# Optimization experiments

Measured on AMD Instinct MI355X. Metric: run time of the kernel, lower is better.

The kernel has to match this reference:

```python
import jax, jax.numpy as jnp
import numpy as np

B, M, ND, ED, D, H = 4, 1024, 64, 8, 64, 4
ALPHA = 0.2
NEG = -9.0e15


def setup_inputs() -> dict:
    key = jax.random.key(0)
    ks = jax.random.split(key, 6)
    h = jax.random.normal(ks[0], (B, M, ND), jnp.float32)
    mch_mask = jax.random.randint(ks[1], (B, M, M), 0, 2).astype(jnp.int32)
    comp_val = jax.random.normal(ks[2], (B, M, M, ED), jnp.float32)
    W = jax.random.normal(ks[3], (H, ND, D), jnp.float32) * 0.1
    W_edge = jax.random.normal(ks[4], (H, ED, D), jnp.float32) * 0.1
    a = jax.random.normal(ks[5], (H, 3 * D), jnp.float32) * 0.1
    return {"h": h, "mch_mask": mch_mask, "comp_val": comp_val,
            "W": W, "W_edge": W_edge, "a": a}


def reference(h, mch_mask, comp_val, W, W_edge, a):
    # h: [B,M,ND], mch_mask: [B,M,M], comp_val: [B,M,M,ED]
    # W: [H,ND,D], W_edge: [H,ED,D], a: [H,3D]  (heads stacked)
    d = W.shape[-1]
    a1, a2, a3 = a[:, :d], a[:, d:2 * d], a[:, 2 * d:]
    Wh = jnp.einsum('bmd,hde->bhme', h, W)              # [B,H,M,D]
    Wh1 = jnp.einsum('bhme,he->bhm', Wh, a1)            # [B,H,M]
    Wh2 = jnp.einsum('bhme,he->bhm', Wh, a2)            # [B,H,M]
    # edge_feas = (comp_val @ W_edge) @ a3, fused: comp_val @ (W_edge @ a3)
    w_e = jnp.einsum('hed,hd->he', W_edge, a3)          # [H,ED]
    edge_feas = jnp.einsum('bkqe,he->bhkq', comp_val, w_e)  # [B,H,M,M]
    e = Wh1[:, :, :, None] + Wh2[:, :, None, :] + edge_feas
    e = jnp.where(e > 0, e, ALPHA * e)                  # leaky_relu
    e = jnp.where(mch_mask[:, None, :, :] > 0, e, NEG)
    attn = jax.nn.softmax(e, axis=-1)                   # [B,H,M,M]
    h_prime = jnp.einsum('bhkq,bhqd->bhkd', attn, Wh)   # [B,H,M,D]
    b, nh, m, dd = h_prime.shape
    return h_prime.transpose(0, 2, 1, 3).reshape(b, m, nh * dd)  # concat heads
```

## Files before the change

### kernel.cpp

```cpp
#include <hip/hip_runtime.h>
#include <hip/hip_bf16.h>

typedef float v4f __attribute__((ext_vector_type(4)));

#define B_ 4
#define M_ 1024
#define ND_ 64
#define ED_ 8
#define D_ 64
#define H_ 4
#define KT 8
#define QC 64
#define NCH (M_ / QC)
#define ALPHA 0.2f

#define WS_WH1 1048576
#define WS_WH2 1064960

#define WHL_F (QC * 256)
#define PB_H 520
#define PB_F (H_ * PB_H)
#define LDS_BYTES ((WHL_F + PB_F + 32 + 32) * 4)

__device__ __forceinline__ v4f splat(float s) { return (v4f){s, s, s, s}; }

__device__ __forceinline__ v4f f4fma(v4f a, v4f b, v4f c) {
#if __has_builtin(__builtin_elementwise_fma)
    return __builtin_elementwise_fma(a, b, c);
#else
    v4f r;
    r.x = fmaf(a.x, b.x, c.x);
    r.y = fmaf(a.y, b.y, c.y);
    r.z = fmaf(a.z, b.z, c.z);
    r.w = fmaf(a.w, b.w, c.w);
    return r;
#endif
}

__global__ __launch_bounds__(256) void k_pre(const float* __restrict__ hg,
                                             const float* __restrict__ Wg,
                                             const float* __restrict__ ag,
                                             float* __restrict__ Whg,
                                             float* __restrict__ Wh1g,
                                             float* __restrict__ Wh2g) {
    __shared__ float wl[ND_ * D_];
    __shared__ float hl[16 * 68];
    const int t = threadIdx.x, lane = t & 63, wv = t >> 6;
    const int bid = blockIdx.x;
    const int b = bid >> 8, h = (bid >> 6) & (H_ - 1), mb = bid & 63;
    const int m0 = mb * 16;

    {
        const float* wsrc = Wg + h * ND_ * D_;
#pragma unroll
        for (int i = 0; i < 4; ++i) {
            const float* s = wsrc + (wv * 4 + i) * 256 + lane * 4;
            __builtin_amdgcn_global_load_lds(
                (const __attribute__((address_space(1))) void*)s,
                (__attribute__((address_space(3))) void*)(wl + (wv * 4 + i) * 256), 16, 0, 0);
        }
    }
    {
        const int mh = t >> 4, u = t & 15;
        v4f hv = *(const v4f*)(hg + ((size_t)(b * M_) + m0 + mh) * ND_ + u * 4);
        *(v4f*)(hl + mh * 68 + u * 4) = hv;
    }
    __syncthreads();

    const int m = t >> 4, d4 = t & 15;
    v4f acc = {0.f, 0.f, 0.f, 0.f};
#pragma unroll
    for (int i = 0; i < ND_; ++i) {
        v4f w4 = *(const v4f*)(wl + i * 64 + d4 * 4);
        float hs = hl[m * 68 + i];
        acc = f4fma(splat(hs), w4, acc);
    }
    *(v4f*)(Whg + (((size_t)(b * H_ + h)) * M_ + m0 + m) * D_ + d4 * 4) = acc;

    v4f a1 = *(const v4f*)(ag + h * 192 + d4 * 4);
    v4f a2 = *(const v4f*)(ag + h * 192 + 64 + d4 * 4);
    v4f p1 = acc * a1, p2 = acc * a2;
    float r1 = (p1.x + p1.y) + (p1.z + p1.w);
    float r2 = (p2.x + p2.y) + (p2.z + p2.w);
#pragma unroll
    for (int off = 8; off >= 1; off >>= 1) {
        r1 += __shfl_xor(r1, off);
        r2 += __shfl_xor(r2, off);
    }
    if (d4 == 0) {
        Wh1g[((size_t)(b * H_ + h)) * M_ + m0 + m] = r1;
        Wh2g[((size_t)(b * H_ + h)) * M_ + m0 + m] = r2;
    }
}

__global__ __launch_bounds__(512, 4) void k_main(const float* __restrict__ cvg,
                                                 const int* __restrict__ mg,
                                                 const float* __restrict__ Whg,
                                                 const float* __restrict__ Wh1g,
                                                 const float* __restrict__ Wh2g,
                                                 const float* __restrict__ Weg,
                                                 const float* __restrict__ ag,
                                                 float* __restrict__ outg) {
    extern __shared__ float smem[];
    float* whl = smem;
    float* pb = smem + WHL_F;
    float* wel = pb + PB_F;
    float* sl = wel + 32;

    const int t = threadIdx.x, lane = t & 63, wv = t >> 6;
    const int nid = (blockIdx.x & 7) * 64 + (blockIdx.x >> 3);
    const int b = nid >> 7;
    const int k0 = (nid & 127) * KT;
    const int hh = lane >> 4, d4 = lane & 15;

    if (t < 32) {
        const int h = t >> 3, e = t & 7;
        const float* wrow = Weg + (h * ED_ + e) * D_;
        const float* a3 = ag + h * 192 + 128;
        float a = 0.f;
#pragma unroll
        for (int i = 0; i < D_; ++i) a = fmaf(wrow[i], a3[i], a);
        wel[t] = a;
    }

    const int ek = k0 + wv;
    float wh1r[H_];
#pragma unroll
    for (int h = 0; h < H_; ++h) wh1r[h] = Wh1g[(b * H_ + h) * M_ + ek];

    const v4f* cvrow = (const v4f*)(cvg + (size_t)(b * M_ + ek) * M_ * ED_);
    const int* mrow = mg + (size_t)(b * M_ + ek) * M_;

    v4f acc[KT];
#pragma unroll
    for (int k = 0; k < KT; ++k) acc[k] = (v4f){0.f, 0.f, 0.f, 0.f};
    float sreg[H_] = {0.f, 0.f, 0.f, 0.f};

#pragma unroll
    for (int i = 0; i < KT; ++i) {
        const int q = wv * KT + i;
        const float* src = Whg + ((size_t)(b * H_ + hh) * M_ + q) * D_ + d4 * 4;
        __builtin_amdgcn_global_load_lds((const __attribute__((address_space(1))) void*)src,
                                         (__attribute__((address_space(3))) void*)(whl + q * 256),
                                         16, 0, 0);
    }
    v4f cv0 = cvrow[lane * 2], cv1 = cvrow[lane * 2 + 1];
    int mk = mrow[lane];
    float wh2r[H_];
#pragma unroll
    for (int h = 0; h < H_; ++h) wh2r[h] = Wh2g[(b * H_ + h) * M_ + lane];
    __syncthreads();

    for (int c = 0; c < NCH; ++c) {
#pragma unroll
        for (int h = 0; h < H_; ++h) {
            v4f wa = *(const v4f*)(wel + h * 8);
            v4f wb = *(const v4f*)(wel + h * 8 + 4);
            v4f tt = cv0 * wa + cv1 * wb;
            float ef = (tt.x + tt.y) + (tt.z + tt.w);
            float e = wh1r[h] + wh2r[h] + ef;
            e = fmaxf(e, ALPHA * e);
            float p = (mk > 0) ? __expf(e) : 0.0f;
            pb[h * PB_H + wv * QC + lane] = p;
            sreg[h] += p;
        }
        __syncthreads();

        if (c + 1 < NCH) {
            const int qn = (c + 1) * QC + lane;
            cv0 = cvrow[qn * 2];
            cv1 = cvrow[qn * 2 + 1];
            mk = mrow[qn];
#pragma unroll
            for (int h = 0; h < H_; ++h) wh2r[h] = Wh2g[(b * H_ + h) * M_ + qn];
        }

        {
            const int q0 = wv * 8;
#pragma unroll
            for (int qq = 0; qq < 2; ++qq) {
                const int q = q0 + qq * 4;
                const v4f w0 = *(const v4f*)(whl + (q + 0) * 256 + lane * 4);
                const v4f w1 = *(const v4f*)(whl + (q + 1) * 256 + lane * 4);
                const v4f w2 = *(const v4f*)(whl + (q + 2) * 256 + lane * 4);
                const v4f w3 = *(const v4f*)(whl + (q + 3) * 256 + lane * 4);
                const float* pbase = pb + hh * PB_H + q;
#pragma unroll
                for (int k = 0; k < KT; ++k) {
                    const v4f pq = *(const v4f*)(pbase + k * 64);
                    v4f a = acc[k];
                    a = f4fma(splat(pq.x), w0, a);
                    a = f4fma(splat(pq.y), w1, a);
                    a = f4fma(splat(pq.z), w2, a);
                    a = f4fma(splat(pq.w), w3, a);
                    acc[k] = a;
                }
            }
        }
        __syncthreads();

        if (c + 1 < NCH) {
#pragma unroll
            for (int i = 0; i < KT; ++i) {
                const int q = wv * KT + i;
                const float* src =
                    Whg + ((size_t)(b * H_ + hh) * M_ + (c + 1) * QC + q) * D_ + d4 * 4;
                __builtin_amdgcn_global_load_lds(
                    (const __attribute__((address_space(1))) void*)src,
                    (__attribute__((address_space(3))) void*)(whl + q * 256), 16, 0, 0);
            }
        }
    }

#pragma unroll
    for (int h = 0; h < H_; ++h) {
        float r = sreg[h];
#pragma unroll
        for (int off = 32; off >= 1; off >>= 1) r += __shfl_xor(r, off);
        if (lane == 0) sl[wv * H_ + h] = r;
    }
#pragma unroll
    for (int k = 0; k < KT; ++k)
        *(v4f*)(whl + (wv * KT + k) * 256 + lane * 4) = acc[k];
    __syncthreads();
    {
        v4f r = (v4f){0.f, 0.f, 0.f, 0.f};
#pragma unroll
        for (int p = 0; p < 8; ++p)
            r += *(const v4f*)(whl + (p * KT + wv) * 256 + lane * 4);
        const float inv = 1.0f / sl[wv * H_ + hh];
        r *= splat(inv);
        *(v4f*)(outg + (size_t)(b * M_ + k0 + wv) * (H_ * D_) + lane * 4) = r;
    }
}

extern "C" void kernel_launch(void* const* d_in, const int* in_sizes, int n_in,
                              void* d_out, int out_size, void* d_ws, size_t ws_size,
                              hipStream_t stream) {
    const float* hg = (const float*)d_in[0];
    const int* mg = (const int*)d_in[1];
    const float* cvg = (const float*)d_in[2];
    const float* Wg = (const float*)d_in[3];
    const float* Weg = (const float*)d_in[4];
    const float* ag = (const float*)d_in[5];
    float* outg = (float*)d_out;
    float* ws = (float*)d_ws;
    float* Whg = ws;
    float* Wh1g = ws + WS_WH1;
    float* Wh2g = ws + WS_WH2;

    (void)hipFuncSetAttribute((const void*)k_main,
                              hipFuncAttributeMaxDynamicSharedMemorySize, LDS_BYTES);

    k_pre<<<1024, 256, 0, stream>>>(hg, Wg, ag, Whg, Wh1g, Wh2g);
    k_main<<<512, 512, LDS_BYTES, stream>>>(cvg, mg, Whg, Wh1g, Wh2g, Weg, ag, outg);
}
```

Baseline: 252.6 us.

## Read Wh directly from global into registers and double-buffer probability LDS

Stops staging Wh tiles in LDS through async global_load_lds. Each thread now loads its eight Wh rows straight from global/L2 into registers every chunk. The probability buffer is double-buffered, which removes one __syncthreads per chunk. Wh1/Wh2 are stored head-minor so a single v4f load fetches all four heads, and the final cross-wave reduction uses a smaller scratch in two passes to shrink LDS. The trade-off is redundant global loads of Wh across waves, plus possible extra latency that is no longer hidden by LDS prefetch.

```diff
diff --git a/kernel.cpp b/kernel.cpp
--- a/kernel.cpp
+++ b/kernel.cpp
@@ -17,10 +17,8 @@
 #define WS_WH1 1048576
 #define WS_WH2 1064960
 
-#define WHL_F (QC * 256)
 #define PB_H 520
 #define PB_F (H_ * PB_H)
-#define LDS_BYTES ((WHL_F + PB_F + 32 + 32) * 4)
 
 __device__ __forceinline__ v4f splat(float s) { return (v4f){s, s, s, s}; }
 
@@ -88,8 +86,8 @@
         r2 += __shfl_xor(r2, off);
     }
     if (d4 == 0) {
-        Wh1g[((size_t)(b * H_ + h)) * M_ + m0 + m] = r1;
-        Wh2g[((size_t)(b * H_ + h)) * M_ + m0 + m] = r2;
+        Wh1g[((size_t)(b * M_) + m0 + m) * H_ + h] = r1;
+        Wh2g[((size_t)(b * M_) + m0 + m) * H_ + h] = r2;
     }
 }
 
@@ -101,11 +99,10 @@
                                                  const float* __restrict__ Weg,
                                                  const float* __restrict__ ag,
                                                  float* __restrict__ outg) {
-    extern __shared__ float smem[];
-    float* whl = smem;
-    float* pb = smem + WHL_F;
-    float* wel = pb + PB_F;
-    float* sl = wel + 32;
+    __shared__ float pb[2 * PB_F];
+    __shared__ float scr[32 * 256];
+    __shared__ float wel[32];
+    __shared__ float sl[32];
 
     const int t = threadIdx.x, lane = t & 63, wv = t >> 6;
     const int nid = (blockIdx.x & 7) * 64 + (blockIdx.x >> 3);
@@ -124,44 +121,34 @@
     }
 
     const int ek = k0 + wv;
-    float wh1r[H_];
-#pragma unroll
-    for (int h = 0; h < H_; ++h) wh1r[h] = Wh1g[(b * H_ + h) * M_ + ek];
-
+    const v4f wh1r = *(const v4f*)(Wh1g + (size_t)(b * M_ + ek) * H_);
     const v4f* cvrow = (const v4f*)(cvg + (size_t)(b * M_ + ek) * M_ * ED_);
     const int* mrow = mg + (size_t)(b * M_ + ek) * M_;
+    const int q0 = wv * 8;
+    const float* whb = Whg + ((size_t)(b * H_ + hh) * M_) * D_ + d4 * 4;
 
     v4f acc[KT];
 #pragma unroll
     for (int k = 0; k < KT; ++k) acc[k] = (v4f){0.f, 0.f, 0.f, 0.f};
     float sreg[H_] = {0.f, 0.f, 0.f, 0.f};
 
-#pragma unroll
-    for (int i = 0; i < KT; ++i) {
-        const int q = wv * KT + i;
-        const float* src = Whg + ((size_t)(b * H_ + hh) * M_ + q) * D_ + d4 * 4;
-        __builtin_amdgcn_global_load_lds((const __attribute__((address_space(1))) void*)src,
-                                         (__attribute__((address_space(3))) void*)(whl + q * 256),
-                                         16, 0, 0);
-    }
     v4f cv0 = cvrow[lane * 2], cv1 = cvrow[lane * 2 + 1];
     int mk = mrow[lane];
-    float wh2r[H_];
-#pragma unroll
-    for (int h = 0; h < H_; ++h) wh2r[h] = Wh2g[(b * H_ + h) * M_ + lane];
+    v4f wh2v = *(const v4f*)(Wh2g + (size_t)(b * M_ + lane) * H_);
     __syncthreads();
 
     for (int c = 0; c < NCH; ++c) {
+        float* pbw = pb + (c & 1) * PB_F;
 #pragma unroll
         for (int h = 0; h < H_; ++h) {
             v4f wa = *(const v4f*)(wel + h * 8);
             v4f wb = *(const v4f*)(wel + h * 8 + 4);
             v4f tt = cv0 * wa + cv1 * wb;
             float ef = (tt.x + tt.y) + (tt.z + tt.w);
-            float e = wh1r[h] + wh2r[h] + ef;
+            float e = wh1r[h] + wh2v[h] + ef;
             e = fmaxf(e, ALPHA * e);
             float p = (mk > 0) ? __expf(e) : 0.0f;
-            pb[h * PB_H + wv * QC + lane] = p;
+            pbw[h * PB_H + wv * QC + lane] = p;
             sreg[h] += p;
         }
         __syncthreads();
@@ -171,45 +158,29 @@
             cv0 = cvrow[qn * 2];
             cv1 = cvrow[qn * 2 + 1];
             mk = mrow[qn];
-#pragma unroll
-            for (int h = 0; h < H_; ++h) wh2r[h] = Wh2g[(b * H_ + h) * M_ + qn];
+            wh2v = *(const v4f*)(Wh2g + (size_t)(b * M_ + qn) * H_);
         }
 
         {
-            const int q0 = wv * 8;
+            const float* whc = whb + (size_t)(c * QC + q0) * D_;
+            v4f w[8];
+#pragma unroll
+            for (int j = 0; j < 8; ++j) w[j] = *(const v4f*)(whc + (size_t)j * D_);
+            const float* pbr = pbw + hh * PB_H + q0;
 #pragma unroll
             for (int qq = 0; qq < 2; ++qq) {
-                const int q = q0 + qq * 4;
-                const v4f w0 = *(const v4f*)(whl + (q + 0) * 256 + lane * 4);
-                const v4f w1 = *(const v4f*)(whl + (q + 1) * 256 + lane * 4);
-                const v4f w2 = *(const v4f*)(whl + (q + 2) * 256 + lane * 4);
-                const v4f w3 = *(const v4f*)(whl + (q + 3) * 256 + lane * 4);
-                const float* pbase = pb + hh * PB_H + q;
 #pragma unroll
                 for (int k = 0; k < KT; ++k) {
-                    const v4f pq = *(const v4f*)(pbase + k * 64);
+                    const v4f pq = *(const v4f*)(pbr + k * QC + qq * 4);
                     v4f a = acc[k];
-                    a = f4fma(splat(pq.x), w0, a);
-                    a = f4fma(splat(pq.y), w1, a);
-                    a = f4fma(splat(pq.z), w2, a);
-                    a = f4fma(splat(pq.w), w3, a);
+                    a = f4fma(splat(pq.x), w[qq * 4 + 0], a);
+                    a = f4fma(splat(pq.y), w[qq * 4 + 1], a);
+                    a = f4fma(splat(pq.z), w[qq * 4 + 2], a);
+                    a = f4fma(splat(pq.w), w[qq * 4 + 3], a);
                     acc[k] = a;
                 }
             }
         }
-        __syncthreads();
-
-        if (c + 1 < NCH) {
-#pragma unroll
-            for (int i = 0; i < KT; ++i) {
-                const int q = wv * KT + i;
-                const float* src =
-                    Whg + ((size_t)(b * H_ + hh) * M_ + (c + 1) * QC + q) * D_ + d4 * 4;
-                __builtin_amdgcn_global_load_lds(
-                    (const __attribute__((address_space(1))) void*)src,
-                    (__attribute__((address_space(3))) void*)(whl + q * 256), 16, 0, 0);
-            }
-        }
     }
 
 #pragma unroll
@@ -220,16 +191,26 @@
         if (lane == 0) sl[wv * H_ + h] = r;
     }
 #pragma unroll
-    for (int k = 0; k < KT; ++k)
-        *(v4f*)(whl + (wv * KT + k) * 256 + lane * 4) = acc[k];
-    __syncthreads();
-    {
+    for (int k = 0; k < 4; ++k) *(v4f*)(scr + (wv * 4 + k) * 256 + lane * 4) = acc[k];
+    __syncthreads();
+    if (wv < 4) {
         v4f r = (v4f){0.f, 0.f, 0.f, 0.f};
 #pragma unroll
         for (int p = 0; p < 8; ++p)
-            r += *(const v4f*)(whl + (p * KT + wv) * 256 + lane * 4);
-        const float inv = 1.0f / sl[wv * H_ + hh];
-        r *= splat(inv);
+            r += *(const v4f*)(scr + (p * 4 + wv) * 256 + lane * 4);
+        r *= splat(1.0f / sl[wv * H_ + hh]);
+        *(v4f*)(outg + (size_t)(b * M_ + k0 + wv) * (H_ * D_) + lane * 4) = r;
+    }
+    __syncthreads();
+#pragma unroll
+    for (int k = 0; k < 4; ++k) *(v4f*)(scr + (wv * 4 + k) * 256 + lane * 4) = acc[4 + k];
+    __syncthreads();
+    if (wv >= 4) {
+        v4f r = (v4f){0.f, 0.f, 0.f, 0.f};
+#pragma unroll
+        for (int p = 0; p < 8; ++p)
+            r += *(const v4f*)(scr + (p * 4 + (wv - 4)) * 256 + lane * 4);
+        r *= splat(1.0f / sl[wv * H_ + hh]);
         *(v4f*)(outg + (size_t)(b * M_ + k0 + wv) * (H_ * D_) + lane * 4) = r;
     }
 }
@@ -249,9 +230,6 @@
     float* Wh1g = ws + WS_WH1;
     float* Wh2g = ws + WS_WH2;
 
-    (void)hipFuncSetAttribute((const void*)k_main,
-                              hipFuncAttributeMaxDynamicSharedMemorySize, LDS_BYTES);
-
     k_pre<<<1024, 256, 0, stream>>>(hg, Wg, ag, Whg, Wh1g, Wh2g);
-    k_main<<<512, 512, LDS_BYTES, stream>>>(cvg, mg, Whg, Wh1g, Wh2g, Weg, ag, outg);
-}
+    k_main<<<512, 512, 0, stream>>>(cvg, mg, Whg, Wh1g, Wh2g, Weg, ag, outg);
+}
```

After: 247.5 us. 1.02x faster.
